# Performance work log

Measured on AMD Instinct MI355X. Metric: run time of the kernel, lower is better.

## Reference

```python
import jax, jax.numpy as jnp
import numpy as np

D = 2048
NH = 16
DH = D // NH          # 128
DC = D // 4           # 512  (KV latent)
DCQ = D // 2          # 1024 (Q latent)
B = 1
L = 2048
MAX_LEN = 4096


def precompute_rope(dh, max_len):
    inv_freq = 1.0 / (10000.0 ** (jnp.arange(0, dh, 2, dtype=jnp.float32) / dh))
    t = jnp.arange(max_len, dtype=jnp.float32)
    freqs = jnp.outer(t, inv_freq)                 # [max_len, dh/2]
    emb = jnp.concatenate([freqs, freqs], axis=-1) # [max_len, dh]
    return jnp.cos(emb), jnp.sin(emb)


def apply_rope(t, cos, sin):
    # t: [B, H, L, dh]; cos/sin: [L, dh]
    x1, x2 = jnp.split(t, 2, axis=-1)
    rot = jnp.concatenate([-x2, x1], axis=-1)
    return t * cos + rot * sin


def setup_inputs() -> dict:
    key = jax.random.key(0)
    ks = jax.random.split(key, 9)
    s = 0.02
    return {
        "x": jax.random.normal(ks[0], (B, L, D), dtype=jnp.float32),
        "W_DKV": jax.random.normal(ks[1], (D, DC), dtype=jnp.float32) * s,
        "W_UK": jax.random.normal(ks[2], (DC, NH * DH), dtype=jnp.float32) * s,
        "W_UV": jax.random.normal(ks[3], (DC, NH * DH), dtype=jnp.float32) * s,
        "W_DQ": jax.random.normal(ks[4], (D, DCQ), dtype=jnp.float32) * s,
        "W_UQ": jax.random.normal(ks[5], (DCQ, 2 * NH * DH), dtype=jnp.float32) * s,
        "W_lam": jax.random.normal(ks[6], (D, NH), dtype=jnp.float32) * s,
        "b_lam": jnp.zeros((NH,), dtype=jnp.float32),
        "W_out": jax.random.normal(ks[7], (D, D), dtype=jnp.float32) * s,
    }


def reference(x, W_DKV, W_UK, W_UV, W_DQ, W_UQ, W_lam, b_lam, W_out):
    Bx, Lx, Dx = x.shape
    cos, sin = precompute_rope(DH, MAX_LEN)
    cos, sin = cos[:Lx], sin[:Lx]

    # MLA KV compression: single K/V shared by the paired query heads
    c_kv = x @ W_DKV                                            # [B, L, dc]
    k = (c_kv @ W_UK).reshape(Bx, Lx, NH, DH).transpose(0, 2, 1, 3)   # [B, nh, L, dh]
    v = (c_kv @ W_UV).reshape(Bx, Lx, NH, DH).transpose(0, 2, 1, 3)   # [B, nh, L, dh]

    # Low-rank Q, doubled heads for differential attention
    c_q = x @ W_DQ                                              # [B, L, dcq]
    q = (c_q @ W_UQ).reshape(Bx, Lx, 2 * NH, DH).transpose(0, 2, 1, 3)  # [B, 2nh, L, dh]

    q = apply_rope(q, cos, sin)
    k = apply_rope(k, cos, sin)

    # Group paired heads (2i, 2i+1) share k/v head i -> avoid repeat_interleave
    qp = q.reshape(Bx, NH, 2, Lx, DH)                           # [B, nh, 2, L, dh]
    scale = 1.0 / jnp.sqrt(jnp.asarray(DH, dtype=x.dtype))
    scores = jnp.einsum('bhpqd,bhkd->bhpqk', qp, k) * scale     # [B, nh, 2, L, L]
    causal = jnp.tril(jnp.ones((Lx, Lx), dtype=bool))
    scores = jnp.where(causal, scores, jnp.asarray(-jnp.inf, dtype=scores.dtype))
    probs = jax.nn.softmax(scores, axis=-1)
    attn = jnp.einsum('bhpqk,bhkd->bhpqd', probs, v)            # [B, nh, 2, L, dh]
    attn1, attn2 = attn[:, :, 0], attn[:, :, 1]                 # [B, nh, L, dh]

    # Token-specific sigmoid lambda per head
    lam = jax.nn.sigmoid(x @ W_lam + b_lam)                     # [B, L, nh]
    lam = lam.transpose(0, 2, 1)[..., None]                     # [B, nh, L, 1]

    out = (attn1 - lam * attn2).transpose(0, 2, 1, 3).reshape(Bx, Lx, Dx)
    return out @ W_out
```

## Files before the change

### kernel.cpp

```cpp
#include <hip/hip_runtime.h>
#include <cstdint>
#include <cstddef>

typedef __bf16 bf16x8 __attribute__((ext_vector_type(8)));
typedef __bf16 bf16x4 __attribute__((ext_vector_type(4)));
typedef float f32x4 __attribute__((ext_vector_type(4)));


template <int N> __device__ __forceinline__ void waitcnt_vm() {
  if constexpr (N == 3)      asm volatile("s_waitcnt vmcnt(3)" ::: "memory");
  else if constexpr (N == 4) asm volatile("s_waitcnt vmcnt(4)" ::: "memory");
  else if constexpr (N == 6) asm volatile("s_waitcnt vmcnt(6)" ::: "memory");
  else if constexpr (N == 8) asm volatile("s_waitcnt vmcnt(8)" ::: "memory");
  else                       asm volatile("s_waitcnt vmcnt(0)" ::: "memory");
}

template <int BM, int NKS>
__device__ __forceinline__ void gemm_core(const __bf16* __restrict__ A,
                                          const __bf16* __restrict__ Bt,
                                          int K, int bm, int bn,
                                          __bf16* As, __bf16* Bs,
                                          f32x4 (*acc)[4]) {
  const int tid = threadIdx.x;
  const int w = tid >> 6;
  const int lane = tid & 63;
  const int quad = lane >> 4;
  const int l16 = lane & 15;
  constexpr int WM = (BM == 128) ? 64 : 32;
  constexpr int MI = WM / 16;
  constexpr int NL = NKS * (BM / 64 + 2);
  const int wm = (w & 1) * WM;
  const int wn = (w >> 1) * 64;
  const int srow = lane >> 2;
  const int sseg = (lane & 3) * 8;

  auto stage = [&](int k0, int buf) {
#pragma unroll
    for (int ks = 0; ks < NKS; ++ks) {
#pragma unroll
      for (int g = 0; g < BM / 64; ++g) {
        const int grp = w + g * 4;
        const __bf16* ga = A + (size_t)(bm + grp * 16 + srow) * K + k0 + ks * 32 + sseg;
        __builtin_amdgcn_global_load_lds(
            (const __attribute__((address_space(1))) void*)ga,
            (__attribute__((address_space(3))) void*)&As[(buf * NKS + ks) * (BM * 32) + grp * 512],
            16, 0, 0);
      }
#pragma unroll
      for (int g = 0; g < 2; ++g) {
        const int grp = w + g * 4;
        const __bf16* gb = Bt + (size_t)(bn + grp * 16 + srow) * K + k0 + ks * 32 + sseg;
        __builtin_amdgcn_global_load_lds(
            (const __attribute__((address_space(1))) void*)gb,
            (__attribute__((address_space(3))) void*)&Bs[(buf * NKS + ks) * 4096 + grp * 512],
            16, 0, 0);
      }
    }
  };

#pragma unroll
  for (int i = 0; i < MI; ++i)
#pragma unroll
    for (int j = 0; j < 4; ++j) acc[i][j] = (f32x4){0.f, 0.f, 0.f, 0.f};

  asm volatile("s_waitcnt vmcnt(0)" ::: "memory");
  stage(0, 0);

  const int NIT = K / (32 * NKS);
  for (int it = 0; it < NIT; ++it) {
    const int cur = it & 1;
    if (it + 1 < NIT) {
      stage((it + 1) * 32 * NKS, cur ^ 1);
      waitcnt_vm<NL>();
    } else {
      waitcnt_vm<0>();
    }
    __builtin_amdgcn_s_barrier();
    asm volatile("" ::: "memory");
    const __bf16* Ab = &As[cur * NKS * (BM * 32)];
    const __bf16* Bb = &Bs[cur * NKS * 4096];
#pragma unroll
    for (int ks = 0; ks < NKS; ++ks) {
      bf16x8 af[MI], bfr[4];
#pragma unroll
      for (int i = 0; i < MI; ++i)
        af[i] = *(const bf16x8*)&Ab[ks * (BM * 32) + (wm + i * 16 + l16) * 32 + quad * 8];
#pragma unroll
      for (int j = 0; j < 4; ++j)
        bfr[j] = *(const bf16x8*)&Bb[ks * 4096 + (wn + j * 16 + l16) * 32 + quad * 8];
#pragma unroll
      for (int i = 0; i < MI; ++i)
#pragma unroll
        for (int j = 0; j < 4; ++j)
          acc[i][j] = __builtin_amdgcn_mfma_f32_16x16x32_bf16(af[i], bfr[j],
                                                              acc[i][j], 0, 0, 0);
    }
    asm volatile("s_waitcnt lgkmcnt(0)" ::: "memory");
    __builtin_amdgcn_s_barrier();
    asm volatile("" ::: "memory");
  }
}

template <int BM, int NKS, bool BF16OUT>
__device__ __forceinline__ void gemm_body(const __bf16* __restrict__ A,
                                          const __bf16* __restrict__ Bt,
                                          void* __restrict__ Cv,
                                          int N, int K, int bm, int bn,
                                          __bf16* As, __bf16* Bs) {
  constexpr int MI = (BM == 128) ? 4 : 2;
  constexpr int WM = (BM == 128) ? 64 : 32;
  f32x4 acc[MI][4];
  gemm_core<BM, NKS>(A, Bt, K, bm, bn, As, Bs, acc);
  const int tid = threadIdx.x;
  const int w = tid >> 6, lane = tid & 63, quad = lane >> 4, l16 = lane & 15;
  const int wm = (w & 1) * WM, wn = (w >> 1) * 64;
#pragma unroll
  for (int i = 0; i < MI; ++i)
#pragma unroll
    for (int j = 0; j < 4; ++j)
#pragma unroll
      for (int r = 0; r < 4; ++r) {
        const int row = bm + wm + i * 16 + quad * 4 + r;
        const int col = bn + wn + j * 16 + l16;
        if constexpr (BF16OUT)
          ((__bf16*)Cv)[(size_t)row * N + col] = (__bf16)acc[i][j][r];
        else
          ((float*)Cv)[(size_t)row * N + col] = acc[i][j][r];
      }
}

template <int BM, int NKS, bool BF16OUT>
__global__ __launch_bounds__(256) void gemm_mfma(const __bf16* __restrict__ A,
                                                 const __bf16* __restrict__ Bt,
                                                 void* __restrict__ Cv,
                                                 int M, int N, int K) {
  __shared__ __bf16 As[2 * BM * 32 * NKS];
  __shared__ __bf16 Bs[2 * 128 * 32 * NKS];
  gemm_body<BM, NKS, BF16OUT>(A, Bt, Cv, N, K, blockIdx.y * BM, blockIdx.x * 128, As, Bs);
}

__device__ __forceinline__ void transpose_tile(const float* __restrict__ src,
                                               __bf16* __restrict__ dst,
                                               int K, int N, int kx, int ny,
                                               float (*T)[36], int tid) {
  const int k0 = kx * 32;
  const int n0 = ny * 32;
  const int r = tid >> 3;
  const int c = (tid & 7) * 4;
  *(float4*)&T[r][c] = *(const float4*)&src[(size_t)(k0 + r) * N + n0 + c];
  __syncthreads();
  bf16x4 o = {(__bf16)T[c + 0][r], (__bf16)T[c + 1][r],
              (__bf16)T[c + 2][r], (__bf16)T[c + 3][r]};
  *(bf16x4*)&dst[(size_t)(n0 + r) * K + k0 + c] = o;
}

__global__ __launch_bounds__(256) void down_lam(
    const __bf16* __restrict__ x_bf, const __bf16* __restrict__ WtDKV,
    const __bf16* __restrict__ WtDQ, __bf16* __restrict__ c_kv,
    __bf16* __restrict__ c_q, const __bf16* __restrict__ WlT,
    const float* __restrict__ b_lam, float* __restrict__ lam,
    const float* __restrict__ W_UK, const float* __restrict__ W_UV,
    const float* __restrict__ W_UQ, __bf16* __restrict__ tUK,
    __bf16* __restrict__ tUV, __bf16* __restrict__ tUQ,
    float* __restrict__ cosT, float* __restrict__ sinT) {
  __shared__ __bf16 As[2 * 64 * 32 * 2];
  __shared__ __bf16 Bs[2 * 128 * 32 * 2];
  int id = blockIdx.x;
  const int tid = threadIdx.x;
  if (id < 416) {
    const int bxl = id >> 5, by = id & 31;
    if (bxl == 12) {
      const int w = tid >> 6, lane = tid & 63, quad = lane >> 4, l16 = lane & 15;
      const int m0 = (by * 4 + w) * 16;
      const __bf16* xrow = x_bf + (size_t)(m0 + l16) * 2048 + quad * 8;
      const __bf16* wrow = WlT + (size_t)l16 * 2048 + quad * 8;
      f32x4 acc[4];
#pragma unroll
      for (int u = 0; u < 4; ++u) acc[u] = (f32x4){0.f, 0.f, 0.f, 0.f};
      for (int k0 = 0; k0 < 2048; k0 += 128) {
#pragma unroll
        for (int u = 0; u < 4; ++u) {
          bf16x8 a = *(const bf16x8*)&xrow[k0 + u * 32];
          bf16x8 b = *(const bf16x8*)&wrow[k0 + u * 32];
          acc[u] = __builtin_amdgcn_mfma_f32_16x16x32_bf16(a, b, acc[u], 0, 0, 0);
        }
      }
      const float bl = b_lam[l16];
#pragma unroll
      for (int r = 0; r < 4; ++r) {
        const float v = acc[0][r] + acc[1][r] + acc[2][r] + acc[3][r] + bl;
        lam[(size_t)(m0 + quad * 4 + r) * 16 + l16] = 1.0f / (1.0f + __expf(-v));
      }
      return;
    }
    if (bxl < 4)
      gemm_body<64, 2, true>(x_bf, WtDKV, (void*)c_kv, 512, 2048,
                             by * 64, bxl * 128, As, Bs);
    else
      gemm_body<64, 2, true>(x_bf, WtDQ, (void*)c_q, 1024, 2048,
                             by * 64, (bxl - 4) * 128, As, Bs);
    return;
  }
  id -= 416;
  if (id < 6144) {
    float (*T)[36] = (float(*)[36])As;
    if (id < 1024)
      transpose_tile(W_UK, tUK, 512, 2048, id & 15, id >> 4, T, tid);
    else if (id < 2048) {
      id -= 1024;
      transpose_tile(W_UV, tUV, 512, 2048, id & 15, id >> 4, T, tid);
    } else {
      id -= 2048;
      transpose_tile(W_UQ, tUQ, 1024, 4096, id & 31, id >> 5, T, tid);
    }
    return;
  }
  id -= 6144;
  {
    const int l = id * 2 + (tid >> 7);
    const int d = tid & 127;
    const int j = d & 63;
    const float inv = exp2f(-(float)j * 0.2076205059304601f);
    const float ang = (float)l * inv;
    cosT[l * 128 + d] = cosf(ang);
    sinT[l * 128 + d] = sinf(ang);
  }
}

__global__ __launch_bounds__(256) void up_fused3(
    const __bf16* __restrict__ c_kv, const __bf16* __restrict__ WtUK,
    const __bf16* __restrict__ WtUV, const __bf16* __restrict__ c_q,
    const __bf16* __restrict__ WtUQ, __bf16* __restrict__ k_bf,
    __bf16* __restrict__ v_t, __bf16* __restrict__ q_bf,
    const float* __restrict__ cosT, const float* __restrict__ sinT) {
  __shared__ __align__(16) char usm[32768];
  __bf16* As = (__bf16*)usm;
  __bf16* Bs = (__bf16*)(usm + 16384);
  const int bx = blockIdx.x;
  const int bm = blockIdx.y * 128;
  const int tid = threadIdx.x;
  const int w = tid >> 6, lane = tid & 63, quad = lane >> 4, l16 = lane & 15;
  const int wm = (w & 1) * 64, wn = (w >> 1) * 64;
  f32x4 acc[4][4];
  if (bx < 16) {
    const int bn = bx * 128;
    gemm_core<128, 1>(c_kv, WtUK, 512, bm, bn, As, Bs, acc);
    __bf16 (*Kt)[128] = (__bf16(*)[128])usm;
#pragma unroll
    for (int i = 0; i < 4; ++i)
#pragma unroll
      for (int j = 0; j < 4; ++j)
#pragma unroll
        for (int r = 0; r < 4; ++r)
          Kt[wm + i * 16 + quad * 4 + r][wn + j * 16 + l16] = (__bf16)acc[i][j][r];
    __syncthreads();
#pragma unroll
    for (int j = 0; j < 4; ++j) {
      const int d = wn + j * 16 + l16;
      const float sgn = (d < 64) ? -1.f : 1.f;
#pragma unroll
      for (int i = 0; i < 4; ++i)
#pragma unroll
        for (int r = 0; r < 4; ++r) {
          const int lr = wm + i * 16 + quad * 4 + r;
          const int l = bm + lr;
          const float v = (float)Kt[lr][d];
          const float pr = (float)Kt[lr][d ^ 64];
          const float ov = v * cosT[l * 128 + d] + sgn * pr * sinT[l * 128 + d];
          k_bf[(size_t)l * 2048 + bn + d] = (__bf16)ov;
        }
    }
  } else if (bx < 32) {
    const int bn = (bx - 16) * 128;
    gemm_core<128, 1>(c_kv, WtUV, 512, bm, bn, As, Bs, acc);
#pragma unroll
    for (int i = 0; i < 4; ++i)
#pragma unroll
      for (int j = 0; j < 4; ++j) {
        const int d = bn + wn + j * 16 + l16;
        const int l = bm + wm + i * 16 + quad * 4;
        bf16x4 pk = {(__bf16)acc[i][j][0], (__bf16)acc[i][j][1],
                     (__bf16)acc[i][j][2], (__bf16)acc[i][j][3]};
        *(bf16x4*)&v_t[(size_t)d * 2048 + l] = pk;
      }
  } else {
    const int bn = (bx - 32) * 128;
    gemm_core<128, 1>(c_q, WtUQ, 1024, bm, bn, As, Bs, acc);
#pragma unroll
    for (int i = 0; i < 4; ++i)
#pragma unroll
      for (int j = 0; j < 4; ++j)
#pragma unroll
        for (int r = 0; r < 4; ++r) {
          const int row = bm + wm + i * 16 + quad * 4 + r;
          const int col = bn + wn + j * 16 + l16;
          q_bf[(size_t)row * 4096 + col] = (__bf16)acc[i][j][r];
        }
  }
}

__global__ __launch_bounds__(256) void prep_all(
    const float* __restrict__ W_DKV, const float* __restrict__ W_DQ,
    const float* __restrict__ x,     const float* __restrict__ W_lam,
    __bf16* __restrict__ tDKV, __bf16* __restrict__ tDQ,
    __bf16* __restrict__ x_bf, __bf16* __restrict__ WlT) {
  __shared__ float T[32][36];
  int t = blockIdx.x;
  const int tid = threadIdx.x;
  if (t < 3072) {
    if (t < 1024)
      transpose_tile(W_DKV, tDKV, 2048, 512, t & 63, t >> 6, T, tid);
    else {
      t -= 1024;
      transpose_tile(W_DQ, tDQ, 2048, 1024, t & 63, t >> 6, T, tid);
    }
    return;
  }
  t -= 3072;
  if (t < 4096) {
    const int i = t * 256 + tid;
    float4 v = *(const float4*)&x[(size_t)i * 4];
    bf16x4 o = {(__bf16)v.x, (__bf16)v.y, (__bf16)v.z, (__bf16)v.w};
    *(bf16x4*)&x_bf[(size_t)i * 4] = o;
    return;
  }
  t -= 4096;
  {
    const int i = t * 256 + tid;
    const int k = i >> 4, n = i & 15;
    WlT[(size_t)n * 2048 + k] = (__bf16)W_lam[i];
  }
}

__global__ __launch_bounds__(512, 2) void attn_kernel3(
    const __bf16* __restrict__ Qb, const __bf16* __restrict__ Kb,
    const __bf16* __restrict__ Vt, const float* __restrict__ cosT,
    const float* __restrict__ sinT, const float* __restrict__ lam,
    __bf16* __restrict__ y, const float* __restrict__ W_out,
    __bf16* __restrict__ Wt_out) {
  __shared__ __align__(16) char smem[81920];
  float (*Ex)[132] = (float(*)[132])smem;

  const int bx = blockIdx.x;
  const int tid = threadIdx.x;
  if (bx >= 512) {
    const int t = (bx - 512) * 2 + (tid >> 8);
    const int st = tid & 255;
    float (*T)[36] = (float(*)[36])(smem + (tid >> 8) * 4608);
    const int k0 = (t & 63) * 32;
    const int n0 = (t >> 6) * 32;
    const int r = st >> 3;
    const int c = (st & 7) * 4;
    *(float4*)&T[r][c] = *(const float4*)&W_out[(size_t)(k0 + r) * 2048 + n0 + c];
    __syncthreads();
    bf16x4 o = {(__bf16)T[c + 0][r], (__bf16)T[c + 1][r],
                (__bf16)T[c + 2][r], (__bf16)T[c + 3][r]};
    *(bf16x4*)&Wt_out[(size_t)(n0 + r) * 2048 + k0 + c] = o;
    return;
  }
  const int hv = bx >> 8;
  const int ii = bx & 255;
  const int qt = hv ? (ii >> 4) : 31 - (ii >> 4);
  const int hk = ii & 15;
  const int q0 = qt * 64;
  const int w = tid >> 6, lane = tid & 63, quad = lane >> 4, l16 = lane & 15;
  const int wrow = (w & 3) * 16;
  const int qoff = (2 * hk + (w >> 2)) * 128;
  const int kvoff = hk * 128;
  const float qscale = 0.08838834764831845f;
  char* Pw = smem + 65536 + w * 2048;

  bf16x8 aq[4];
  {
    const int l = q0 + wrow + l16;
    const size_t qbase = (size_t)l * 4096 + qoff + quad * 8;
    bf16x8 raw[4];
#pragma unroll
    for (int ks = 0; ks < 4; ++ks)
      raw[ks] = *(const bf16x8*)&Qb[qbase + ks * 32];
#pragma unroll
    for (int ks = 0; ks < 4; ++ks) {
      const float* cp = &cosT[l * 128 + ks * 32 + quad * 8];
      const float* sp = &sinT[l * 128 + ks * 32 + quad * 8];
#pragma unroll
      for (int j = 0; j < 8; ++j) {
        const float cv = cp[j];
        const float sv = sp[j];
        const float rot = (ks < 2) ? -(float)raw[ks + 2][j] : (float)raw[ks - 2][j];
        aq[ks][j] = (__bf16)(((float)raw[ks][j] * cv + rot * sv) * qscale);
      }
    }
  }

  auto stage = [&](int kt_, char* buf) {
    const int k0_ = kt_ * 64;
    __bf16* Ksb = (__bf16*)buf;
    __bf16* Vsb = (__bf16*)(buf + 16384);
#pragma unroll
    for (int d = 0; d < 2; ++d) {
      const int r0 = w * 8 + d * 4;
      const int row = r0 + (lane >> 4);
      const int ck = (lane & 15) ^ (row & 15);
      const __bf16* ga = Kb + (size_t)(k0_ + row) * 2048 + kvoff + ck * 8;
      __builtin_amdgcn_global_load_lds(
          (const __attribute__((address_space(1))) void*)ga,
          (__attribute__((address_space(3))) void*)&Ksb[r0 * 128], 16, 0, 0);
      const int r0v = w * 16 + d * 8;
      const int rowv = r0v + (lane >> 3);
      const int cv = (lane & 7) ^ (rowv & 7);
      const __bf16* gv = Vt + (size_t)(kvoff + rowv) * 2048 + k0_ + cv * 8;
      __builtin_amdgcn_global_load_lds(
          (const __attribute__((address_space(1))) void*)gv,
          (__attribute__((address_space(3))) void*)&Vsb[r0v * 64], 16, 0, 0);
    }
  };

  f32x4 o[8];
#pragma unroll
  for (int i = 0; i < 8; ++i) o[i] = (f32x4){0.f, 0.f, 0.f, 0.f};
  float m = -1e30f, lsum = 0.f;

  asm volatile("s_waitcnt vmcnt(0)" ::: "memory");
  stage(0, smem);

  for (int kt = 0; kt <= qt; ++kt) {
    const int cur = kt & 1;
    __bf16* Ks = (__bf16*)(smem + cur * 32768);
    __bf16* Vs = (__bf16*)(smem + cur * 32768 + 16384);
    const int k0 = kt * 64;
    if (kt < qt) {
      stage(kt + 1, smem + (cur ^ 1) * 32768);
      asm volatile("s_waitcnt vmcnt(4)" ::: "memory");
    } else {
      asm volatile("s_waitcnt vmcnt(0)" ::: "memory");
    }
    __builtin_amdgcn_s_barrier();
    asm volatile("" ::: "memory");
    f32x4 st[4];
#pragma unroll
    for (int t = 0; t < 4; ++t) st[t] = (f32x4){0.f, 0.f, 0.f, 0.f};
    __builtin_amdgcn_s_setprio(1);
#pragma unroll
    for (int ks = 0; ks < 4; ++ks) {
#pragma unroll
      for (int t = 0; t < 4; ++t) {
        bf16x8 ak = *(bf16x8*)&Ks[(t * 16 + l16) * 128 + (((ks * 4 + quad) ^ l16) << 3)];
        st[t] = __builtin_amdgcn_mfma_f32_16x16x32_bf16(ak, aq[ks], st[t], 0, 0, 0);
      }
    }
    __builtin_amdgcn_s_setprio(0);
    {
      const int q = q0 + wrow + l16;
      float rm = -1e30f;
      if (kt != qt) {
#pragma unroll
        for (int t = 0; t < 4; ++t)
#pragma unroll
          for (int r = 0; r < 4; ++r) rm = fmaxf(rm, st[t][r]);
      } else {
#pragma unroll
        for (int t = 0; t < 4; ++t)
#pragma unroll
          for (int r = 0; r < 4; ++r) {
            const int key = k0 + t * 16 + quad * 4 + r;
            if (key > q) st[t][r] = -1e30f;
            rm = fmaxf(rm, st[t][r]);
          }
      }
      rm = fmaxf(rm, __shfl_xor(rm, 16, 64));
      rm = fmaxf(rm, __shfl_xor(rm, 32, 64));
      const float mn = fmaxf(m, rm);
      float rs = 0.f;
#pragma unroll
      for (int t = 0; t < 4; ++t)
#pragma unroll
        for (int r = 0; r < 4; ++r) {
          st[t][r] = __expf(st[t][r] - mn);
          rs += st[t][r];
        }
      rs += __shfl_xor(rs, 16, 64);
      rs += __shfl_xor(rs, 32, 64);
      if (__any(rm > m)) {
        const float alpha = __expf(m - mn);
        lsum = lsum * alpha + rs;
        m = mn;
#pragma unroll
        for (int r = 0; r < 4; ++r) {
          const float ar = __shfl(alpha, quad * 4 + r, 64);
#pragma unroll
          for (int nt = 0; nt < 8; ++nt) o[nt][r] *= ar;
        }
      } else {
        lsum += rs;
      }
      const int prow = l16;
#pragma unroll
      for (int t = 0; t < 4; ++t) {
        bf16x4 pk = {(__bf16)st[t][0], (__bf16)st[t][1],
                     (__bf16)st[t][2], (__bf16)st[t][3]};
        const int wch = (t * 2 + (quad >> 1)) ^ (prow & 7);
        *(bf16x4*)(Pw + prow * 128 + wch * 16 + (quad & 1) * 8) = pk;
      }
    }
    __builtin_amdgcn_s_setprio(1);
#pragma unroll
    for (int ks = 0; ks < 2; ++ks) {
      const int rch = ((ks * 4 + quad) ^ (l16 & 7)) << 4;
      bf16x8 pa = *(bf16x8*)(Pw + l16 * 128 + rch);
#pragma unroll
      for (int nt = 0; nt < 8; ++nt) {
        bf16x8 bv = *(bf16x8*)&Vs[(nt * 16 + l16) * 64 + (((ks * 4 + quad) ^ (l16 & 7)) << 3)];
        o[nt] = __builtin_amdgcn_mfma_f32_16x16x32_bf16(pa, bv, o[nt], 0, 0, 0);
      }
    }
    __builtin_amdgcn_s_setprio(0);
    asm volatile("s_waitcnt lgkmcnt(0)" ::: "memory");
    __builtin_amdgcn_s_barrier();
    asm volatile("" ::: "memory");
  }
  const float linv = 1.0f / lsum;
  if (w >= 4) {
#pragma unroll
    for (int r = 0; r < 4; ++r) {
      const float inv = __shfl(linv, quad * 4 + r, 64);
      const int rr = wrow + quad * 4 + r;
#pragma unroll
      for (int nt = 0; nt < 8; ++nt)
        Ex[rr][nt * 16 + l16] = o[nt][r] * inv;
    }
  }
  __syncthreads();
  if (w < 4) {
#pragma unroll
    for (int r = 0; r < 4; ++r) {
      const float inv = __shfl(linv, quad * 4 + r, 64);
      const int rr = wrow + quad * 4 + r;
      const int l = q0 + rr;
      const float lm = lam[l * 16 + hk];
      __bf16* dst = y + (size_t)l * 2048 + hk * 128;
#pragma unroll
      for (int nt = 0; nt < 8; ++nt) {
        const float v1 = o[nt][r] * inv;
        dst[nt * 16 + l16] = (__bf16)(v1 - lm * Ex[rr][nt * 16 + l16]);
      }
    }
  }
}

extern "C" void kernel_launch(void* const* d_in, const int* in_sizes, int n_in,
                              void* d_out, int out_size, void* d_ws, size_t ws_size,
                              hipStream_t stream) {
  const float* x     = (const float*)d_in[0];
  const float* W_DKV = (const float*)d_in[1];
  const float* W_UK  = (const float*)d_in[2];
  const float* W_UV  = (const float*)d_in[3];
  const float* W_DQ  = (const float*)d_in[4];
  const float* W_UQ  = (const float*)d_in[5];
  const float* W_lam = (const float*)d_in[6];
  const float* b_lam = (const float*)d_in[7];
  const float* W_out = (const float*)d_in[8];
  float* out = (float*)d_out;

  char* ws = (char*)d_ws;
  #define MB(n) ((size_t)(n) << 20)
  __bf16* x_bf   = (__bf16*)(ws + MB(0));
  __bf16* Wt_DKV = (__bf16*)(ws + MB(8));
  __bf16* Wt_DQ  = (__bf16*)(ws + MB(10));
  __bf16* c_kv   = (__bf16*)(ws + MB(14));
  __bf16* c_q    = (__bf16*)(ws + MB(16));
  __bf16* Wt_UK  = (__bf16*)(ws + MB(20));
  __bf16* Wt_UV  = (__bf16*)(ws + MB(22));
  __bf16* Wt_UQ  = (__bf16*)(ws + MB(24));
  __bf16* k_bf   = (__bf16*)(ws + MB(32));
  __bf16* y_bf   = (__bf16*)(ws + MB(40));
  __bf16* q_bf   = (__bf16*)(ws + MB(48));
  __bf16* v_t    = (__bf16*)(ws + MB(64));
  float*  lam    = (float*)(ws + MB(88));
  float*  cosT   = (float*)(ws + MB(89));
  float*  sinT   = (float*)(ws + MB(90));
  __bf16* WlT    = (__bf16*)(ws + MB(91));
  __bf16* Wt_out = (__bf16*)(ws + MB(92));

  prep_all<<<7296, 256, 0, stream>>>(W_DKV, W_DQ, x, W_lam,
                                     Wt_DKV, Wt_DQ, x_bf, WlT);
  down_lam<<<7584, 256, 0, stream>>>(x_bf, Wt_DKV, Wt_DQ, c_kv, c_q,
                                     WlT, b_lam, lam,
                                     W_UK, W_UV, W_UQ, Wt_UK, Wt_UV, Wt_UQ,
                                     cosT, sinT);
  up_fused3<<<dim3(64, 16), 256, 0, stream>>>(c_kv, Wt_UK, Wt_UV, c_q, Wt_UQ,
                                              k_bf, v_t, q_bf, cosT, sinT);
  attn_kernel3<<<2560, 512, 0, stream>>>(q_bf, k_bf, v_t, cosT, sinT, lam,
                                         y_bf, W_out, Wt_out);
  gemm_mfma<64, 2, false><<<dim3(16, 32), 256, 0, stream>>>(y_bf, Wt_out, out, 2048, 2048, 2048);
}
```

Baseline: 288.4 us.

## Use 8-wave blocks for down-projection and output GEMMs, pack transposes two per block

Generalizes the GEMM core to a template warp count and runs the down-projection and output-projection GEMMs with 512-thread blocks, so each wave handles a narrower 32-column slice. The fused down_lam launch moves to 512 threads: each block now does two transpose tiles and four RoPE rows, and the lam branch is remapped to 8 waves. The intent is more waves per tile to hide latency and fewer blocks overall. In exchange, each wave does less MFMA work per LDS fragment load, and the per-wave wait counts become uneven.

```diff
diff --git a/kernel.cpp b/kernel.cpp
--- a/kernel.cpp
+++ b/kernel.cpp
@@ -8,29 +8,31 @@
 
 
 template <int N> __device__ __forceinline__ void waitcnt_vm() {
-  if constexpr (N == 3)      asm volatile("s_waitcnt vmcnt(3)" ::: "memory");
+  if constexpr (N == 2)      asm volatile("s_waitcnt vmcnt(2)" ::: "memory");
+  else if constexpr (N == 3) asm volatile("s_waitcnt vmcnt(3)" ::: "memory");
   else if constexpr (N == 4) asm volatile("s_waitcnt vmcnt(4)" ::: "memory");
   else if constexpr (N == 6) asm volatile("s_waitcnt vmcnt(6)" ::: "memory");
   else if constexpr (N == 8) asm volatile("s_waitcnt vmcnt(8)" ::: "memory");
   else                       asm volatile("s_waitcnt vmcnt(0)" ::: "memory");
 }
 
-template <int BM, int NKS>
+template <int BM, int NKS, int NW>
 __device__ __forceinline__ void gemm_core(const __bf16* __restrict__ A,
                                           const __bf16* __restrict__ Bt,
                                           int K, int bm, int bn,
                                           __bf16* As, __bf16* Bs,
-                                          f32x4 (*acc)[4]) {
+                                          f32x4 (*acc)[128 / ((NW / 2) * 16)]) {
   const int tid = threadIdx.x;
   const int w = tid >> 6;
   const int lane = tid & 63;
   const int quad = lane >> 4;
   const int l16 = lane & 15;
   constexpr int WM = (BM == 128) ? 64 : 32;
+  constexpr int WN = 128 / (NW / 2);
   constexpr int MI = WM / 16;
-  constexpr int NL = NKS * (BM / 64 + 2);
+  constexpr int NJ = WN / 16;
   const int wm = (w & 1) * WM;
-  const int wn = (w >> 1) * 64;
+  const int wn = (w >> 1) * WN;
   const int srow = lane >> 2;
   const int sseg = (lane & 3) * 8;
 
@@ -38,21 +40,19 @@
 #pragma unroll
     for (int ks = 0; ks < NKS; ++ks) {
 #pragma unroll
-      for (int g = 0; g < BM / 64; ++g) {
-        const int grp = w + g * 4;
-        const __bf16* ga = A + (size_t)(bm + grp * 16 + srow) * K + k0 + ks * 32 + sseg;
+      for (int g = w; g < BM / 16; g += NW) {
+        const __bf16* ga = A + (size_t)(bm + g * 16 + srow) * K + k0 + ks * 32 + sseg;
         __builtin_amdgcn_global_load_lds(
             (const __attribute__((address_space(1))) void*)ga,
-            (__attribute__((address_space(3))) void*)&As[(buf * NKS + ks) * (BM * 32) + grp * 512],
+            (__attribute__((address_space(3))) void*)&As[(buf * NKS + ks) * (BM * 32) + g * 512],
             16, 0, 0);
       }
 #pragma unroll
-      for (int g = 0; g < 2; ++g) {
-        const int grp = w + g * 4;
-        const __bf16* gb = Bt + (size_t)(bn + grp * 16 + srow) * K + k0 + ks * 32 + sseg;
+      for (int g = w; g < 8; g += NW) {
+        const __bf16* gb = Bt + (size_t)(bn + g * 16 + srow) * K + k0 + ks * 32 + sseg;
         __builtin_amdgcn_global_load_lds(
             (const __attribute__((address_space(1))) void*)gb,
-            (__attribute__((address_space(3))) void*)&Bs[(buf * NKS + ks) * 4096 + grp * 512],
+            (__attribute__((address_space(3))) void*)&Bs[(buf * NKS + ks) * 4096 + g * 512],
             16, 0, 0);
       }
     }
@@ -61,7 +61,7 @@
 #pragma unroll
   for (int i = 0; i < MI; ++i)
 #pragma unroll
-    for (int j = 0; j < 4; ++j) acc[i][j] = (f32x4){0.f, 0.f, 0.f, 0.f};
+    for (int j = 0; j < NJ; ++j) acc[i][j] = (f32x4){0.f, 0.f, 0.f, 0.f};
 
   asm volatile("s_waitcnt vmcnt(0)" ::: "memory");
   stage(0, 0);
@@ -71,7 +71,12 @@
     const int cur = it & 1;
     if (it + 1 < NIT) {
       stage((it + 1) * 32 * NKS, cur ^ 1);
-      waitcnt_vm<NL>();
+      if constexpr (NW == 4) {
+        waitcnt_vm<NKS * (BM / 64 + 2)>();
+      } else {
+        if (w < BM / 16) waitcnt_vm<NKS * 2>();
+        else             waitcnt_vm<NKS * 1>();
+      }
     } else {
       waitcnt_vm<0>();
     }
@@ -81,17 +86,17 @@
     const __bf16* Bb = &Bs[cur * NKS * 4096];
 #pragma unroll
     for (int ks = 0; ks < NKS; ++ks) {
-      bf16x8 af[MI], bfr[4];
+      bf16x8 af[MI], bfr[NJ];
 #pragma unroll
       for (int i = 0; i < MI; ++i)
         af[i] = *(const bf16x8*)&Ab[ks * (BM * 32) + (wm + i * 16 + l16) * 32 + quad * 8];
 #pragma unroll
-      for (int j = 0; j < 4; ++j)
+      for (int j = 0; j < NJ; ++j)
         bfr[j] = *(const bf16x8*)&Bb[ks * 4096 + (wn + j * 16 + l16) * 32 + quad * 8];
 #pragma unroll
       for (int i = 0; i < MI; ++i)
 #pragma unroll
-        for (int j = 0; j < 4; ++j)
+        for (int j = 0; j < NJ; ++j)
           acc[i][j] = __builtin_amdgcn_mfma_f32_16x16x32_bf16(af[i], bfr[j],
                                                               acc[i][j], 0, 0, 0);
     }
@@ -101,23 +106,25 @@
   }
 }
 
-template <int BM, int NKS, bool BF16OUT>
+template <int BM, int NKS, bool BF16OUT, int NW = 4>
 __device__ __forceinline__ void gemm_body(const __bf16* __restrict__ A,
                                           const __bf16* __restrict__ Bt,
                                           void* __restrict__ Cv,
                                           int N, int K, int bm, int bn,
                                           __bf16* As, __bf16* Bs) {
-  constexpr int MI = (BM == 128) ? 4 : 2;
   constexpr int WM = (BM == 128) ? 64 : 32;
-  f32x4 acc[MI][4];
-  gemm_core<BM, NKS>(A, Bt, K, bm, bn, As, Bs, acc);
+  constexpr int WN = 128 / (NW / 2);
+  constexpr int MI = WM / 16;
+  constexpr int NJ = WN / 16;
+  f32x4 acc[MI][NJ];
+  gemm_core<BM, NKS, NW>(A, Bt, K, bm, bn, As, Bs, acc);
   const int tid = threadIdx.x;
   const int w = tid >> 6, lane = tid & 63, quad = lane >> 4, l16 = lane & 15;
-  const int wm = (w & 1) * WM, wn = (w >> 1) * 64;
+  const int wm = (w & 1) * WM, wn = (w >> 1) * WN;
 #pragma unroll
   for (int i = 0; i < MI; ++i)
 #pragma unroll
-    for (int j = 0; j < 4; ++j)
+    for (int j = 0; j < NJ; ++j)
 #pragma unroll
       for (int r = 0; r < 4; ++r) {
         const int row = bm + wm + i * 16 + quad * 4 + r;
@@ -129,24 +136,24 @@
       }
 }
 
-template <int BM, int NKS, bool BF16OUT>
-__global__ __launch_bounds__(256) void gemm_mfma(const __bf16* __restrict__ A,
-                                                 const __bf16* __restrict__ Bt,
-                                                 void* __restrict__ Cv,
-                                                 int M, int N, int K) {
+template <int BM, int NKS, bool BF16OUT, int NW = 4>
+__global__ __launch_bounds__(NW * 64) void gemm_mfma(const __bf16* __restrict__ A,
+                                                     const __bf16* __restrict__ Bt,
+                                                     void* __restrict__ Cv,
+                                                     int M, int N, int K) {
   __shared__ __bf16 As[2 * BM * 32 * NKS];
   __shared__ __bf16 Bs[2 * 128 * 32 * NKS];
-  gemm_body<BM, NKS, BF16OUT>(A, Bt, Cv, N, K, blockIdx.y * BM, blockIdx.x * 128, As, Bs);
+  gemm_body<BM, NKS, BF16OUT, NW>(A, Bt, Cv, N, K, blockIdx.y * BM, blockIdx.x * 128, As, Bs);
 }
 
 __device__ __forceinline__ void transpose_tile(const float* __restrict__ src,
                                                __bf16* __restrict__ dst,
                                                int K, int N, int kx, int ny,
-                                               float (*T)[36], int tid) {
+                                               float (*T)[36], int st) {
   const int k0 = kx * 32;
   const int n0 = ny * 32;
-  const int r = tid >> 3;
-  const int c = (tid & 7) * 4;
+  const int r = st >> 3;
+  const int c = (st & 7) * 4;
   *(float4*)&T[r][c] = *(const float4*)&src[(size_t)(k0 + r) * N + n0 + c];
   __syncthreads();
   bf16x4 o = {(__bf16)T[c + 0][r], (__bf16)T[c + 1][r],
@@ -154,7 +161,7 @@
   *(bf16x4*)&dst[(size_t)(n0 + r) * K + k0 + c] = o;
 }
 
-__global__ __launch_bounds__(256) void down_lam(
+__global__ __launch_bounds__(512) void down_lam(
     const __bf16* __restrict__ x_bf, const __bf16* __restrict__ WtDKV,
     const __bf16* __restrict__ WtDQ, __bf16* __restrict__ c_kv,
     __bf16* __restrict__ c_q, const __bf16* __restrict__ WlT,
@@ -170,8 +177,9 @@
   if (id < 416) {
     const int bxl = id >> 5, by = id & 31;
     if (bxl == 12) {
+      if (by >= 16) return;
       const int w = tid >> 6, lane = tid & 63, quad = lane >> 4, l16 = lane & 15;
-      const int m0 = (by * 4 + w) * 16;
+      const int m0 = (by * 8 + w) * 16;
       const __bf16* xrow = x_bf + (size_t)(m0 + l16) * 2048 + quad * 8;
       const __bf16* wrow = WlT + (size_t)l16 * 2048 + quad * 8;
       f32x4 acc[4];
@@ -194,30 +202,32 @@
       return;
     }
     if (bxl < 4)
-      gemm_body<64, 2, true>(x_bf, WtDKV, (void*)c_kv, 512, 2048,
-                             by * 64, bxl * 128, As, Bs);
+      gemm_body<64, 2, true, 8>(x_bf, WtDKV, (void*)c_kv, 512, 2048,
+                                by * 64, bxl * 128, As, Bs);
     else
-      gemm_body<64, 2, true>(x_bf, WtDQ, (void*)c_q, 1024, 2048,
-                             by * 64, (bxl - 4) * 128, As, Bs);
+      gemm_body<64, 2, true, 8>(x_bf, WtDQ, (void*)c_q, 1024, 2048,
+                                by * 64, (bxl - 4) * 128, As, Bs);
     return;
   }
   id -= 416;
-  if (id < 6144) {
-    float (*T)[36] = (float(*)[36])As;
-    if (id < 1024)
-      transpose_tile(W_UK, tUK, 512, 2048, id & 15, id >> 4, T, tid);
-    else if (id < 2048) {
-      id -= 1024;
-      transpose_tile(W_UV, tUV, 512, 2048, id & 15, id >> 4, T, tid);
+  if (id < 3072) {
+    int t = id * 2 + (tid >> 8);
+    const int st = tid & 255;
+    float (*T)[36] = (float(*)[36])((char*)As + (tid >> 8) * 4608);
+    if (t < 1024)
+      transpose_tile(W_UK, tUK, 512, 2048, t & 15, t >> 4, T, st);
+    else if (t < 2048) {
+      t -= 1024;
+      transpose_tile(W_UV, tUV, 512, 2048, t & 15, t >> 4, T, st);
     } else {
-      id -= 2048;
-      transpose_tile(W_UQ, tUQ, 1024, 4096, id & 31, id >> 5, T, tid);
+      t -= 2048;
+      transpose_tile(W_UQ, tUQ, 1024, 4096, t & 31, t >> 5, T, st);
     }
     return;
   }
-  id -= 6144;
+  id -= 3072;
   {
-    const int l = id * 2 + (tid >> 7);
+    const int l = id * 4 + (tid >> 7);
     const int d = tid & 127;
     const int j = d & 63;
     const float inv = exp2f(-(float)j * 0.2076205059304601f);
@@ -244,7 +254,7 @@
   f32x4 acc[4][4];
   if (bx < 16) {
     const int bn = bx * 128;
-    gemm_core<128, 1>(c_kv, WtUK, 512, bm, bn, As, Bs, acc);
+    gemm_core<128, 1, 4>(c_kv, WtUK, 512, bm, bn, As, Bs, acc);
     __bf16 (*Kt)[128] = (__bf16(*)[128])usm;
 #pragma unroll
     for (int i = 0; i < 4; ++i)
@@ -272,7 +282,7 @@
     }
   } else if (bx < 32) {
     const int bn = (bx - 16) * 128;
-    gemm_core<128, 1>(c_kv, WtUV, 512, bm, bn, As, Bs, acc);
+    gemm_core<128, 1, 4>(c_kv, WtUV, 512, bm, bn, As, Bs, acc);
 #pragma unroll
     for (int i = 0; i < 4; ++i)
 #pragma unroll
@@ -285,7 +295,7 @@
       }
   } else {
     const int bn = (bx - 32) * 128;
-    gemm_core<128, 1>(c_q, WtUQ, 1024, bm, bn, As, Bs, acc);
+    gemm_core<128, 1, 4>(c_q, WtUQ, 1024, bm, bn, As, Bs, acc);
 #pragma unroll
     for (int i = 0; i < 4; ++i)
 #pragma unroll
@@ -583,7 +593,7 @@
 
   prep_all<<<7296, 256, 0, stream>>>(W_DKV, W_DQ, x, W_lam,
                                      Wt_DKV, Wt_DQ, x_bf, WlT);
-  down_lam<<<7584, 256, 0, stream>>>(x_bf, Wt_DKV, Wt_DQ, c_kv, c_q,
+  down_lam<<<4000, 512, 0, stream>>>(x_bf, Wt_DKV, Wt_DQ, c_kv, c_q,
                                      WlT, b_lam, lam,
                                      W_UK, W_UV, W_UQ, Wt_UK, Wt_UV, Wt_UQ,
                                      cosT, sinT);
@@ -591,5 +601,5 @@
                                               k_bf, v_t, q_bf, cosT, sinT);
   attn_kernel3<<<2560, 512, 0, stream>>>(q_bf, k_bf, v_t, cosT, sinT, lam,
                                          y_bf, W_out, Wt_out);
-  gemm_mfma<64, 2, false><<<dim3(16, 32), 256, 0, stream>>>(y_bf, Wt_out, out, 2048, 2048, 2048);
-}
+  gemm_mfma<64, 2, false, 8><<<dim3(16, 32), 512, 0, stream>>>(y_bf, Wt_out, out, 2048, 2048, 2048);
+}
```

Measured after the change: 278.5 us (median of 2 runs). 1.04x faster.
